# Kernel optimization log

Hardware: AMD Instinct MI355X
Metric: run time of the kernel (lower is better)

The kernel has to match this reference:

```python
import jax, jax.numpy as jnp
import numpy as np

L, D, d, H0, H1, K = 8, 64, 32, 512, 512, 10
EPS = 1e-5

def setup_inputs() -> dict:
    key = jax.random.key(0)
    ks = jax.random.split(key, 14)
    N = 65536
    x = jax.random.normal(ks[0], (N, D + 1), dtype=jnp.float32)  # last col = labels
    def w(k, shape):
        return jax.random.normal(k, shape, dtype=jnp.float32) * 0.05
    inp = {
        'x': x,
        'sW0': w(ks[1], (L, H0, d)),  'sb0': w(ks[2], (L, H0)),
        'sW1': w(ks[3], (L, H1, H0)), 'sb1': w(ks[4], (L, H1)),
        'sW2': w(ks[5], (L, D - d, H1)), 'sb2': w(ks[6], (L, D - d)),
        'tW0': w(ks[7], (L, H0, d)),  'tb0': w(ks[8], (L, H0)),
        'tW1': w(ks[9], (L, H1, H0)), 'tb1': w(ks[10], (L, H1)),
        'tW2': w(ks[11], (L, D - d, H1)), 'tb2': w(ks[12], (L, D - d)),
        'means': jax.random.normal(ks[13], (K, D), dtype=jnp.float32),
    }
    return inp

def _mlp(h, W0, b0, W1, b1, W2, b2):
    h = jax.nn.relu(h @ W0.T + b0)
    h = jax.nn.relu(h @ W1.T + b1)
    return h @ W2.T + b2

def reference(x, sW0, sb0, sW1, sb1, sW2, sb2, tW0, tb0, tW1, tb1, tW2, tb2, means):
    x = x[:, :D]  # drop label column
    det_s = jnp.zeros(x.shape[0], dtype=x.dtype)
    for i in range(L):
        # fresh BatchNorm1d in training mode: batch mean / biased var, weight=1, bias=0
        mu = x.mean(0)
        var = x.var(0)
        x = (x - mu) / jnp.sqrt(var + EPS)
        if i % 2 == 0:  # b1: first d features pass through
            x1, x2 = x[:, :d], x[:, d:]
        else:           # b2: last d features pass through
            x1, x2 = x[:, D - d:], x[:, :D - d]
        s = _mlp(x1, sW0[i], sb0[i], sW1[i], sb1[i], sW2[i], sb2[i])
        t = _mlp(x1, tW0[i], tb0[i], tW1[i], tb1[i], tW2[i], tb2[i])
        y2 = x2 * jnp.exp(s) + t
        det_s = det_s + s.sum(-1)
        x = jnp.concatenate([x1, y2], axis=-1)
    y = x
    # GMM prior: equal weights, identity covariance
    diff = y[:, None, :] - means[None, :, :]            # [N, K, D]
    comp_logp = -0.5 * (jnp.sum(diff * diff, -1) + D * jnp.log(2.0 * jnp.pi))
    log_likelihood = jax.scipy.special.logsumexp(comp_logp - jnp.log(float(K)), axis=-1)
    loss = -1.0 * (det_s + log_likelihood).mean()
    return (y, loss, log_likelihood, det_s, log_likelihood.mean(), det_s.mean())
```

## Files before the change

### kernel.cpp

```cpp
#include <hip/hip_runtime.h>
#include <cstdint>
#include <cstddef>

typedef unsigned short u16;
typedef unsigned int   u32;
typedef __attribute__((ext_vector_type(8))) short short8;
typedef __attribute__((ext_vector_type(4))) float f32x4;

__device__ __forceinline__ float bf2f(u16 b) {
  union { u32 u; float f; } v; v.u = ((u32)b) << 16; return v.f;
}
__device__ __forceinline__ u16 f2bf(float f) {
  union { float f; u32 u; } v; v.f = f;
  u32 u = v.u;
  return (u16)((u + 0x7fffu + ((u >> 16) & 1u)) >> 16);
}
__device__ __forceinline__ u32 pk2(u16 a, u16 b) { return (u32)a | ((u32)b << 16); }

__global__ void detect_dtype(const u16* __restrict__ xin, int* __restrict__ flag) {
  int hits = 0;
  for (int i = threadIdx.x; i < 16384; i += 256) {
    u16 v = xin[i];
    if (((v >> 7) & 0xFF) == 0xFF) hits++;
  }
  if (hits) atomicOr(flag, 1);
}

__global__ __launch_bounds__(256) void convert_bf16(const void* __restrict__ src,
    u16* __restrict__ dst, int n, const int* __restrict__ flag) {
  int i = blockIdx.x * 256 + threadIdx.x;
  if (i >= n) return;
  if (*flag) dst[i] = f2bf(((const float*)src)[i]);
  else       dst[i] = ((const u16*)src)[i];
}

__global__ __launch_bounds__(256) void repack_w0(const void* __restrict__ src,
    u16* __restrict__ dst, const int* __restrict__ flag, int L) {
  int idx = blockIdx.x * 256 + threadIdx.x;
  if (idx >= L * 2048) return;
  int layer = idx >> 11, r = idx & 2047;
  int lane = r & 63, fo = (r >> 6) & 7, w = r >> 9;
  int m = lane & 15, q = lane >> 4;
  int row = w * 128 + fo * 16 + m;
  size_t s = (size_t)layer * 16384 + (size_t)row * 32 + q * 8;
  u16 o[8];
  if (*flag) { const float* p = (const float*)src;
    #pragma unroll
    for (int j = 0; j < 8; ++j) o[j] = f2bf(p[s + j]);
  } else { const u16* p = (const u16*)src;
    #pragma unroll
    for (int j = 0; j < 8; ++j) o[j] = p[s + j];
  }
  *(uint4*)&dst[(size_t)idx * 8] =
      make_uint4(pk2(o[0], o[1]), pk2(o[2], o[3]), pk2(o[4], o[5]), pk2(o[6], o[7]));
}

__global__ __launch_bounds__(256) void repack_w1(const void* __restrict__ src,
    u16* __restrict__ dst, const int* __restrict__ flag, int L) {
  int idx = blockIdx.x * 256 + threadIdx.x;
  if (idx >= L * 32768) return;
  int layer = idx >> 15, r = idx & 32767;
  int lane = r & 63, fo = (r >> 6) & 3, ks = (r >> 8) & 15;
  int oc2 = (r >> 12) & 1, w = (r >> 13) & 3;
  int m = lane & 15, q = lane >> 4;
  int row = w * 128 + oc2 * 64 + fo * 16 + m;
  int col = ks * 32 + q * 8;
  size_t s = (size_t)layer * 262144 + (size_t)row * 512 + col;
  u16 o[8];
  if (*flag) { const float* p = (const float*)src;
    #pragma unroll
    for (int j = 0; j < 8; ++j) o[j] = f2bf(p[s + j]);
  } else { const u16* p = (const u16*)src;
    #pragma unroll
    for (int j = 0; j < 8; ++j) o[j] = p[s + j];
  }
  *(uint4*)&dst[(size_t)idx * 8] =
      make_uint4(pk2(o[0], o[1]), pk2(o[2], o[3]), pk2(o[4], o[5]), pk2(o[6], o[7]));
}

__global__ __launch_bounds__(256) void repack_w2(const void* __restrict__ src,
    u16* __restrict__ dst, const int* __restrict__ flag, int L) {
  int idx = blockIdx.x * 256 + threadIdx.x;
  if (idx >= L * 4096) return;
  int layer = idx >> 12, r = idx & 4095;
  int lane = r & 63, fo2 = (r >> 6) & 1, fo = (r >> 7) & 3;
  int oc2 = (r >> 9) & 1, w = (r >> 10) & 3;
  int m = lane & 15, q = lane >> 4;
  int row = fo2 * 16 + m;
  int col = w * 128 + oc2 * 64 + fo * 16 + q * 8;
  u16 o[8];
  #pragma unroll
  for (int j = 0; j < 8; ++j) {
    int cj = col + j;
    if (cj < 512) {
      size_t s = (size_t)layer * 16384 + (size_t)row * 512 + cj;
      o[j] = (*flag) ? f2bf(((const float*)src)[s]) : ((const u16*)src)[s];
    } else o[j] = 0;
  }
  *(uint4*)&dst[(size_t)idx * 8] =
      make_uint4(pk2(o[0], o[1]), pk2(o[2], o[3]), pk2(o[4], o[5]), pk2(o[6], o[7]));
}

__global__ __launch_bounds__(256) void init_x(const void* __restrict__ xin,
    float* __restrict__ x, const int* __restrict__ flag, int N) {
  int idx = blockIdx.x * 256 + threadIdx.x;
  if (idx >= N * 64) return;
  int n = idx >> 6, c = idx & 63;
  size_t si = (size_t)n * 65 + c;
  float v = (*flag) ? ((const float*)xin)[si] : bf2f(((const u16*)xin)[si]);
  if (!isfinite(v)) v = 0.0f;
  x[idx] = v;
}

__global__ __launch_bounds__(256) void col_stats(const float* __restrict__ x,
                                                 float* __restrict__ stats, int N) {
  int c   = threadIdx.x & 63;
  int sub = threadIdx.x >> 6;
  int rows = N / gridDim.x;
  int r0 = blockIdx.x * rows;
  float s = 0.f, s2 = 0.f;
  for (int r = sub; r < rows; r += 4) {
    float v = x[(size_t)(r0 + r) * 64 + c];
    s += v; s2 = fmaf(v, v, s2);
  }
  __shared__ float ls[256], lq[256];
  ls[threadIdx.x] = s; lq[threadIdx.x] = s2;
  __syncthreads();
  if (threadIdx.x < 64) {
    s  = ls[c] + ls[c + 64] + ls[c + 128] + ls[c + 192];
    s2 = lq[c] + lq[c + 64] + lq[c + 128] + lq[c + 192];
    atomicAdd(&stats[c], s);
    atomicAdd(&stats[64 + c], s2);
  }
}

__global__ __launch_bounds__(256, 2) void fused_layer(
    float* __restrict__ x, float* __restrict__ det,
    const float* __restrict__ statsC, float* __restrict__ statsN,
    const u16* __restrict__ pW0s, const u16* __restrict__ B0s,
    const u16* __restrict__ pW1s, const u16* __restrict__ B1s,
    const u16* __restrict__ pW2s, const u16* __restrict__ B2s,
    const u16* __restrict__ pW0t, const u16* __restrict__ B0t,
    const u16* __restrict__ pW1t, const u16* __restrict__ B1t,
    const u16* __restrict__ pW2t, const u16* __restrict__ B2t,
    int off1, int first, int N)
{
  __shared__ __align__(16) u16 h0s[64 * 512];
  __shared__ __align__(16) u16 xh[6144];
  __shared__ float musr[128];
  __shared__ float csum[64], csqs[64];

  const int tid  = threadIdx.x;
  const int lane = tid & 63, wave = tid >> 6;
  const int m = lane & 15, q = lane >> 4;
  const int mb = m & 7;
  const int r0 = blockIdx.x * 64;
  const int off2 = 32 - off1;
  const float invN = 1.0f / (float)N;

  if (tid < 64) {
    float mu  = statsC[tid] * invN;
    float var = fmaxf(statsC[64 + tid] * invN - mu * mu, 0.0f);
    musr[tid]      = mu;
    musr[64 + tid] = 1.0f / sqrtf(var + 1e-5f);
    csum[tid] = 0.0f; csqs[tid] = 0.0f;
  }
  __syncthreads();

  {
    int row = tid >> 2, kq = (tid & 3) * 8;
    const float* src = x + (size_t)(r0 + row) * 64 + off1 + kq;
    float4 v0 = *(const float4*)src;
    float4 v1 = *(const float4*)(src + 4);
    float vv[8] = {v0.x, v0.y, v0.z, v0.w, v1.x, v1.y, v1.z, v1.w};
    u16 pk[8];
    #pragma unroll
    for (int u_ = 0; u_ < 8; ++u_) {
      int c = off1 + kq + u_;
      pk[u_] = f2bf((vv[u_] - musr[c]) * musr[64 + c]);
    }
    *(uint4*)&xh[row * 40 + kq] =
        make_uint4(pk2(pk[0], pk[1]), pk2(pk[2], pk[3]),
                   pk2(pk[4], pk[5]), pk2(pk[6], pk[7]));
  }
  __syncthreads();

  short8 xb[4];
  #pragma unroll
  for (int fm = 0; fm < 4; ++fm)
    xb[fm] = *(const short8*)&xh[(fm * 16 + m) * 40 + q * 8];

  const u16* W0p[2] = {pW0s, pW0t}; const u16* B0p[2] = {B0s, B0t};
  const u16* W1p[2] = {pW1s, pW1t}; const u16* B1p[2] = {B1s, B1t};
  const u16* W2p[2] = {pW2s, pW2t};

  const f32x4 fz = {0.f, 0.f, 0.f, 0.f};
  f32x4 a2[2][4][2];
  #pragma unroll
  for (int p = 0; p < 2; ++p)
    #pragma unroll
    for (int fr = 0; fr < 4; ++fr)
      #pragma unroll
      for (int fo2 = 0; fo2 < 2; ++fo2) a2[p][fr][fo2] = fz;

  short8 zf;
  #pragma unroll
  for (int j = 0; j < 8; ++j) zf[j] = 0;

  u16* h1w = &xh[wave * 1536];

  #pragma unroll
  for (int p = 0; p < 2; ++p) {
    if (p == 1) __syncthreads();
    const u16 *W0 = W0p[p], *B0 = B0p[p], *W1 = W1p[p], *B1 = B1p[p], *W2 = W2p[p];

    short8 w0n = *(const short8*)(W0 + (size_t)(wave * 8) * 512 + lane * 8);
    #pragma unroll
    for (int fo = 0; fo < 8; ++fo) {
      short8 w0c = w0n;
      int fn = (fo + 1) & 7;
      w0n = *(const short8*)(W0 + (size_t)(wave * 8 + fn) * 512 + lane * 8);
      int colf = wave * 128 + fo * 16;
      int cb = colf + q * 4;
      float bb[4];
      #pragma unroll
      for (int i2 = 0; i2 < 4; ++i2) bb[i2] = bf2f(B0[cb + i2]);
      int gw = cb >> 3, wo = cb & 7;
      #pragma unroll
      for (int fm = 0; fm < 4; ++fm) {
        f32x4 d = __builtin_amdgcn_mfma_f32_16x16x32_bf16(w0c, xb[fm], fz, 0, 0, 0);
        u16 pk[4];
        #pragma unroll
        for (int i2 = 0; i2 < 4; ++i2) pk[i2] = f2bf(fmaxf(d[i2] + bb[i2], 0.0f));
        int row = fm * 16 + m;
        *(uint2*)&h0s[row * 512 + ((gw ^ (row & 7)) << 3) + wo] =
            make_uint2(pk2(pk[0], pk[1]), pk2(pk[2], pk[3]));
      }
    }
    __syncthreads();

    #pragma unroll 1
    for (int oc2 = 0; oc2 < 2; ++oc2) {
      int ocb = wave * 128 + oc2 * 64;
      const u16* W1b = W1 + (size_t)(wave * 2 + oc2) * 32768;
      f32x4 c1[4][4];
      #pragma unroll
      for (int fo = 0; fo < 4; ++fo)
        #pragma unroll
        for (int fm = 0; fm < 4; ++fm) c1[fo][fm] = fz;

      short8 wan[4], bfn[4];
      #pragma unroll
      for (int fm = 0; fm < 4; ++fm)
        bfn[fm] = *(const short8*)&h0s[(fm * 16 + m) * 512 + ((q ^ mb) << 3)];
      #pragma unroll
      for (int fo = 0; fo < 4; ++fo)
        wan[fo] = *(const short8*)(W1b + fo * 512 + lane * 8);

      #pragma unroll 4
      for (int ks = 0; ks < 16; ++ks) {
        short8 wac[4], bfc[4];
        #pragma unroll
        for (int z = 0; z < 4; ++z) { wac[z] = wan[z]; bfc[z] = bfn[z]; }
        int kn = (ks + 1) & 15;
        #pragma unroll
        for (int fm = 0; fm < 4; ++fm)
          bfn[fm] = *(const short8*)&h0s[(fm * 16 + m) * 512 +
                                         ((((kn << 2) | q) ^ mb) << 3)];
        #pragma unroll
        for (int fo = 0; fo < 4; ++fo)
          wan[fo] = *(const short8*)(W1b + (size_t)kn * 2048 + fo * 512 + lane * 8);
        #pragma unroll
        for (int fo = 0; fo < 4; ++fo)
          #pragma unroll
          for (int fm = 0; fm < 4; ++fm)
            c1[fo][fm] = __builtin_amdgcn_mfma_f32_16x16x32_bf16(
                wac[fo], bfc[fm], c1[fo][fm], 0, 0, 0);
      }

      #pragma unroll
      for (int fo = 0; fo < 4; ++fo) {
        int colb = ocb + fo * 16 + q * 4;
        float bb[4];
        #pragma unroll
        for (int i2 = 0; i2 < 4; ++i2) bb[i2] = bf2f(B1[colb + i2]);
        #pragma unroll
        for (int fm = 0; fm < 4; ++fm) {
          u16 pk[4];
          #pragma unroll
          for (int i2 = 0; i2 < 4; ++i2)
            pk[i2] = f2bf(fmaxf(c1[fo][fm][i2] + bb[i2], 0.0f));
          *(uint2*)&h1w[(fm * 16 + m) * 24 + q * 4] =
              make_uint2(pk2(pk[0], pk[1]), pk2(pk[2], pk[3]));
        }
        asm volatile("s_waitcnt lgkmcnt(0)" ::: "memory");
        const u16* W2b = W2 + (size_t)((wave * 2 + oc2) * 8 + fo * 2) * 512;
        #pragma unroll
        for (int fr = 0; fr < 4; ++fr) {
          short8 af = zf;
          if (q < 2) af = *(const short8*)&h1w[(fr * 16 + m) * 24 + q * 8];
          #pragma unroll
          for (int fo2 = 0; fo2 < 2; ++fo2) {
            short8 wf = *(const short8*)(W2b + fo2 * 512 + lane * 8);
            a2[p][fr][fo2] = __builtin_amdgcn_mfma_f32_16x16x32_bf16(
                af, wf, a2[p][fr][fo2], 0, 0, 0);
          }
        }
      }
    }
  }
  __syncthreads();

  float* red = (float*)h0s;
  #pragma unroll
  for (int fr = 0; fr < 4; ++fr)
    #pragma unroll
    for (int fo2 = 0; fo2 < 2; ++fo2)
      #pragma unroll
      for (int i2 = 0; i2 < 4; ++i2) {
        int row = fr * 16 + q * 4 + i2, col = fo2 * 16 + m;
        red[(wave * 64 + row) * 32 + col]       = a2[0][fr][fo2][i2];
        red[((4 + wave) * 64 + row) * 32 + col] = a2[1][fr][fo2][i2];
      }
  __syncthreads();

  {
    int col = tid & 31, rh = tid >> 5;
    float muA = musr[off1 + col], rsA = musr[64 + off1 + col];
    float muB = musr[off2 + col], rsB = musr[64 + off2 + col];
    float b2s = bf2f(B2s[col]), b2t = bf2f(B2t[col]);
    float cs1 = 0.f, cq1 = 0.f, cs2 = 0.f, cq2 = 0.f;
    #pragma unroll
    for (int u_ = 0; u_ < 8; ++u_) {
      int row = u_ * 8 + rh;
      float sv = b2s, tv = b2t;
      #pragma unroll
      for (int w = 0; w < 4; ++w) {
        sv += red[(w * 64 + row) * 32 + col];
        tv += red[((4 + w) * 64 + row) * 32 + col];
      }
      size_t rb = (size_t)(r0 + row) * 64;
      float x1n = (x[rb + off1 + col] - muA) * rsA;
      float x2n = (x[rb + off2 + col] - muB) * rsB;
      float y2 = fmaf(x2n, expf(fminf(sv, 30.0f)), tv);
      x[rb + col]      = x1n;
      x[rb + 32 + col] = y2;
      cs1 += x1n; cq1 = fmaf(x1n, x1n, cq1);
      cs2 += y2;  cq2 = fmaf(y2, y2, cq2);
      float rs_ = sv;
      rs_ += __shfl_xor(rs_, 1);  rs_ += __shfl_xor(rs_, 2);
      rs_ += __shfl_xor(rs_, 4);  rs_ += __shfl_xor(rs_, 8);
      rs_ += __shfl_xor(rs_, 16);
      if (col == 0) {
        int r = r0 + row;
        if (first) det[r] = rs_; else det[r] += rs_;
      }
    }
    cs1 += __shfl_xor(cs1, 32); cq1 += __shfl_xor(cq1, 32);
    cs2 += __shfl_xor(cs2, 32); cq2 += __shfl_xor(cq2, 32);
    if (lane < 32) {
      atomicAdd(&csum[col], cs1);      atomicAdd(&csqs[col], cq1);
      atomicAdd(&csum[32 + col], cs2); atomicAdd(&csqs[32 + col], cq2);
    }
  }
  __syncthreads();
  if (tid < 64) {
    atomicAdd(&statsN[tid],      csum[tid]);
    atomicAdd(&statsN[64 + tid], csqs[tid]);
  }
}

__global__ __launch_bounds__(256) void gmm_out(const float* __restrict__ x,
    const float* __restrict__ det, const u16* __restrict__ means,
    void* __restrict__ outv, double* __restrict__ acc,
    const int* __restrict__ flag, int N) {
  __shared__ float ms[640];
  __shared__ double rll[256], rdt[256];
  for (int i = threadIdx.x; i < 640; i += 256) ms[i] = bf2f(means[i]);
  __syncthreads();
  int of32 = *flag;
  int n = blockIdx.x * 256 + threadIdx.x;
  double llv = 0.0, dtv = 0.0;
  if (n < N) {
    float y[64];
    size_t rb = (size_t)n * 64;
    #pragma unroll
    for (int c = 0; c < 64; ++c) y[c] = x[rb + c];
    if (of32) {
      float* out = (float*)outv;
      #pragma unroll
      for (int c = 0; c < 64; ++c) out[rb + c] = y[c];
    } else {
      u16* out = (u16*)outv;
      #pragma unroll
      for (int c = 0; c < 64; ++c) out[rb + c] = f2bf(y[c]);
    }
    float lp[10];
    float mx = -3.0e38f;
    #pragma unroll
    for (int k = 0; k < 10; ++k) {
      float d2 = 0.0f;
      #pragma unroll
      for (int c = 0; c < 64; ++c) { float d = y[c] - ms[k * 64 + c]; d2 = fmaf(d, d, d2); }
      float v = -0.5f * (d2 + 64.0f * 1.8378770664093455f) - 2.302585092994046f;
      lp[k] = v; mx = fmaxf(mx, v);
    }
    float se = 0.0f;
    #pragma unroll
    for (int k = 0; k < 10; ++k) se += expf(lp[k] - mx);
    float ll = mx + logf(se);
    float dv = det[n];
    size_t NY = (size_t)N * 64;
    if (of32) {
      float* out = (float*)outv;
      out[NY + 1 + n]     = ll;
      out[NY + 1 + N + n] = dv;
    } else {
      u16* out = (u16*)outv;
      out[NY + 1 + n]     = f2bf(ll);
      out[NY + 1 + N + n] = f2bf(dv);
    }
    llv = ll; dtv = dv;
  }
  rll[threadIdx.x] = llv; rdt[threadIdx.x] = dtv;
  __syncthreads();
  for (int st = 128; st > 0; st >>= 1) {
    if (threadIdx.x < st) {
      rll[threadIdx.x] += rll[threadIdx.x + st];
      rdt[threadIdx.x] += rdt[threadIdx.x + st];
    }
    __syncthreads();
  }
  if (threadIdx.x == 0) { atomicAdd(&acc[0], rll[0]); atomicAdd(&acc[1], rdt[0]); }
}

__global__ void finalize(const double* __restrict__ acc, void* __restrict__ outv,
                         const int* __restrict__ flag, int N) {
  double llm = acc[0] / (double)N;
  double dm  = acc[1] / (double)N;
  size_t NY = (size_t)N * 64;
  if (*flag) {
    float* out = (float*)outv;
    out[NY]                         = (float)(-(llm + dm));
    out[NY + 1 + 2 * (size_t)N]     = (float)llm;
    out[NY + 1 + 2 * (size_t)N + 1] = (float)dm;
  } else {
    u16* out = (u16*)outv;
    out[NY]                         = f2bf((float)(-(llm + dm)));
    out[NY + 1 + 2 * (size_t)N]     = f2bf((float)llm);
    out[NY + 1 + 2 * (size_t)N + 1] = f2bf((float)dm);
  }
}

extern "C" void kernel_launch(void* const* d_in, const int* in_sizes, int n_in,
                              void* d_out, int out_size, void* d_ws, size_t ws_size,
                              hipStream_t stream) {
  const int N = in_sizes[0] / 65;
  (void)n_in; (void)out_size; (void)ws_size;

  char* ws = (char*)d_ws;
  size_t off = 0;
  auto alloc = [&](size_t bytes) -> void* {
    void* p = ws + off; off = (off + bytes + 255) & ~(size_t)255; return p;
  };
  int*    flag  = (int*)   alloc(4);
  double* acc   = (double*)alloc(2 * 8);
  float*  stats = (float*) alloc(9 * 128 * 4);
  float*  det   = (float*) alloc((size_t)N * 4);
  float*  x     = (float*) alloc((size_t)N * 64 * 4);

  u16* pW0s = (u16*)alloc((size_t)8 * 16384 * 2);
  u16* pW0t = (u16*)alloc((size_t)8 * 16384 * 2);
  u16* pW1s = (u16*)alloc((size_t)8 * 262144 * 2);
  u16* pW1t = (u16*)alloc((size_t)8 * 262144 * 2);
  u16* pW2s = (u16*)alloc((size_t)8 * 32768 * 2);
  u16* pW2t = (u16*)alloc((size_t)8 * 32768 * 2);

  static const int bcnt[7] = {8*512, 8*512, 8*32, 8*512, 8*512, 8*32, 640};
  static const int bsrc[7] = {2, 4, 6, 8, 10, 12, 13};
  u16* bptr[7];
  for (int t = 0; t < 7; ++t) bptr[t] = (u16*)alloc((size_t)bcnt[t] * 2);

  hipMemsetAsync(flag, 0, 4, stream);
  hipMemsetAsync(stats, 0, 9 * 128 * sizeof(float), stream);
  hipMemsetAsync(acc, 0, 2 * sizeof(double), stream);
  detect_dtype<<<dim3(1), dim3(256), 0, stream>>>((const u16*)d_in[0], flag);
  for (int t = 0; t < 7; ++t) {
    int n = bcnt[t];
    convert_bf16<<<dim3((n + 255) / 256), dim3(256), 0, stream>>>(
        d_in[bsrc[t]], bptr[t], n, flag);
  }
  repack_w0<<<dim3(64),   dim3(256), 0, stream>>>(d_in[1],  pW0s, flag, 8);
  repack_w0<<<dim3(64),   dim3(256), 0, stream>>>(d_in[7],  pW0t, flag, 8);
  repack_w1<<<dim3(1024), dim3(256), 0, stream>>>(d_in[3],  pW1s, flag, 8);
  repack_w1<<<dim3(1024), dim3(256), 0, stream>>>(d_in[9],  pW1t, flag, 8);
  repack_w2<<<dim3(128),  dim3(256), 0, stream>>>(d_in[5],  pW2s, flag, 8);
  repack_w2<<<dim3(128),  dim3(256), 0, stream>>>(d_in[11], pW2t, flag, 8);

  const int NE = N * 64;
  init_x<<<dim3((NE + 255) / 256), dim3(256), 0, stream>>>(d_in[0], x, flag, N);
  col_stats<<<dim3(256), dim3(256), 0, stream>>>(x, stats, N);

  for (int i = 0; i < 8; ++i) {
    fused_layer<<<dim3(N / 64), dim3(256), 0, stream>>>(
        x, det, stats + (size_t)i * 128, stats + (size_t)(i + 1) * 128,
        pW0s + (size_t)i * 16384,  bptr[0] + (size_t)i * 512,
        pW1s + (size_t)i * 262144, bptr[1] + (size_t)i * 512,
        pW2s + (size_t)i * 32768,  bptr[2] + (size_t)i * 32,
        pW0t + (size_t)i * 16384,  bptr[3] + (size_t)i * 512,
        pW1t + (size_t)i * 262144, bptr[4] + (size_t)i * 512,
        pW2t + (size_t)i * 32768,  bptr[5] + (size_t)i * 32,
        (i & 1) ? 32 : 0, (i == 0) ? 1 : 0, N);
  }

  gmm_out<<<dim3((N + 255) / 256), dim3(256), 0, stream>>>(x, det, bptr[6],
                                                           d_out, acc, flag, N);
  finalize<<<dim3(1), dim3(1), 0, stream>>>(acc, d_out, flag, N);
}
```

Measured before the change: 1.136 ms.

## Split hidden-layer K dimension to halve LDS and raise occupancy to three blocks

The first hidden layer's activations are now computed in two halves of 256 columns, each consumed right away by the second-layer GEMM. This shrinks the LDS buffer for h0 from 64x512 to 64x256. The s-network output is merged and stored to LDS as bf16 before the t-network runs, so the two-pass accumulators no longer stay live in registers. Launch bounds go from 2 to 3 blocks per CU, the W0 repack matches the new half-split order, and the software prefetch of W1 and h0 fragments is dropped. Extra barriers, W0 recomputation of the x tile, and rounding s to bf16 are the trade-offs.

```diff
diff --git a/kernel.cpp b/kernel.cpp
--- a/kernel.cpp
+++ b/kernel.cpp
@@ -39,9 +39,10 @@
   int idx = blockIdx.x * 256 + threadIdx.x;
   if (idx >= L * 2048) return;
   int layer = idx >> 11, r = idx & 2047;
-  int lane = r & 63, fo = (r >> 6) & 7, w = r >> 9;
+  int lane = r & 63, f = r >> 6;
+  int kh = f >> 4, w = (f >> 2) & 3, fo = f & 3;
   int m = lane & 15, q = lane >> 4;
-  int row = w * 128 + fo * 16 + m;
+  int row = kh * 256 + w * 64 + fo * 16 + m;
   size_t s = (size_t)layer * 16384 + (size_t)row * 32 + q * 8;
   u16 o[8];
   if (*flag) { const float* p = (const float*)src;
@@ -134,7 +135,7 @@
   }
 }
 
-__global__ __launch_bounds__(256, 2) void fused_layer(
+__global__ __launch_bounds__(256, 3) void fused_layer(
     float* __restrict__ x, float* __restrict__ det,
     const float* __restrict__ statsC, float* __restrict__ statsN,
     const u16* __restrict__ pW0s, const u16* __restrict__ B0s,
@@ -145,8 +146,10 @@
     const u16* __restrict__ pW2t, const u16* __restrict__ B2t,
     int off1, int first, int N)
 {
-  __shared__ __align__(16) u16 h0s[64 * 512];
-  __shared__ __align__(16) u16 xh[6144];
+  __shared__ __align__(16) u16 h0h[64 * 256];
+  __shared__ __align__(16) u16 x1s[2560];
+  __shared__ __align__(16) u16 h1wA[4096];
+  __shared__ __align__(16) u16 sst[2048];
   __shared__ float musr[128];
   __shared__ float csum[64], csqs[64];
 
@@ -179,103 +182,91 @@
       int c = off1 + kq + u_;
       pk[u_] = f2bf((vv[u_] - musr[c]) * musr[64 + c]);
     }
-    *(uint4*)&xh[row * 40 + kq] =
+    *(uint4*)&x1s[row * 40 + kq] =
         make_uint4(pk2(pk[0], pk[1]), pk2(pk[2], pk[3]),
                    pk2(pk[4], pk[5]), pk2(pk[6], pk[7]));
   }
-  __syncthreads();
-
-  short8 xb[4];
-  #pragma unroll
-  for (int fm = 0; fm < 4; ++fm)
-    xb[fm] = *(const short8*)&xh[(fm * 16 + m) * 40 + q * 8];
 
   const u16* W0p[2] = {pW0s, pW0t}; const u16* B0p[2] = {B0s, B0t};
   const u16* W1p[2] = {pW1s, pW1t}; const u16* B1p[2] = {B1s, B1t};
   const u16* W2p[2] = {pW2s, pW2t};
 
   const f32x4 fz = {0.f, 0.f, 0.f, 0.f};
-  f32x4 a2[2][4][2];
-  #pragma unroll
-  for (int p = 0; p < 2; ++p)
-    #pragma unroll
-    for (int fr = 0; fr < 4; ++fr)
-      #pragma unroll
-      for (int fo2 = 0; fo2 < 2; ++fo2) a2[p][fr][fo2] = fz;
-
   short8 zf;
   #pragma unroll
   for (int j = 0; j < 8; ++j) zf[j] = 0;
 
-  u16* h1w = &xh[wave * 1536];
-
-  #pragma unroll
+  u16* h1w = &h1wA[wave * 1024];
+  float* mergef = (float*)h0h;
+
   for (int p = 0; p < 2; ++p) {
-    if (p == 1) __syncthreads();
     const u16 *W0 = W0p[p], *B0 = B0p[p], *W1 = W1p[p], *B1 = B1p[p], *W2 = W2p[p];
-
-    short8 w0n = *(const short8*)(W0 + (size_t)(wave * 8) * 512 + lane * 8);
-    #pragma unroll
-    for (int fo = 0; fo < 8; ++fo) {
-      short8 w0c = w0n;
-      int fn = (fo + 1) & 7;
-      w0n = *(const short8*)(W0 + (size_t)(wave * 8 + fn) * 512 + lane * 8);
-      int colf = wave * 128 + fo * 16;
-      int cb = colf + q * 4;
-      float bb[4];
-      #pragma unroll
-      for (int i2 = 0; i2 < 4; ++i2) bb[i2] = bf2f(B0[cb + i2]);
-      int gw = cb >> 3, wo = cb & 7;
-      #pragma unroll
-      for (int fm = 0; fm < 4; ++fm) {
-        f32x4 d = __builtin_amdgcn_mfma_f32_16x16x32_bf16(w0c, xb[fm], fz, 0, 0, 0);
-        u16 pk[4];
-        #pragma unroll
-        for (int i2 = 0; i2 < 4; ++i2) pk[i2] = f2bf(fmaxf(d[i2] + bb[i2], 0.0f));
-        int row = fm * 16 + m;
-        *(uint2*)&h0s[row * 512 + ((gw ^ (row & 7)) << 3) + wo] =
-            make_uint2(pk2(pk[0], pk[1]), pk2(pk[2], pk[3]));
-      }
-    }
-    __syncthreads();
+    f32x4 a2[4][2];
+    #pragma unroll
+    for (int fr = 0; fr < 4; ++fr)
+      #pragma unroll
+      for (int fo2 = 0; fo2 < 2; ++fo2) a2[fr][fo2] = fz;
 
     #pragma unroll 1
     for (int oc2 = 0; oc2 < 2; ++oc2) {
-      int ocb = wave * 128 + oc2 * 64;
-      const u16* W1b = W1 + (size_t)(wave * 2 + oc2) * 32768;
+      const int ocb = wave * 128 + oc2 * 64;
       f32x4 c1[4][4];
       #pragma unroll
       for (int fo = 0; fo < 4; ++fo)
         #pragma unroll
         for (int fm = 0; fm < 4; ++fm) c1[fo][fm] = fz;
 
-      short8 wan[4], bfn[4];
-      #pragma unroll
-      for (int fm = 0; fm < 4; ++fm)
-        bfn[fm] = *(const short8*)&h0s[(fm * 16 + m) * 512 + ((q ^ mb) << 3)];
-      #pragma unroll
-      for (int fo = 0; fo < 4; ++fo)
-        wan[fo] = *(const short8*)(W1b + fo * 512 + lane * 8);
-
-      #pragma unroll 4
-      for (int ks = 0; ks < 16; ++ks) {
-        short8 wac[4], bfc[4];
-        #pragma unroll
-        for (int z = 0; z < 4; ++z) { wac[z] = wan[z]; bfc[z] = bfn[z]; }
-        int kn = (ks + 1) & 15;
-        #pragma unroll
-        for (int fm = 0; fm < 4; ++fm)
-          bfn[fm] = *(const short8*)&h0s[(fm * 16 + m) * 512 +
-                                         ((((kn << 2) | q) ^ mb) << 3)];
-        #pragma unroll
-        for (int fo = 0; fo < 4; ++fo)
-          wan[fo] = *(const short8*)(W1b + (size_t)kn * 2048 + fo * 512 + lane * 8);
-        #pragma unroll
-        for (int fo = 0; fo < 4; ++fo)
+      #pragma unroll 1
+      for (int kh = 0; kh < 2; ++kh) {
+        __syncthreads();
+        {
+          short8 xb[4];
           #pragma unroll
           for (int fm = 0; fm < 4; ++fm)
-            c1[fo][fm] = __builtin_amdgcn_mfma_f32_16x16x32_bf16(
-                wac[fo], bfc[fm], c1[fo][fm], 0, 0, 0);
+            xb[fm] = *(const short8*)&x1s[(fm * 16 + m) * 40 + q * 8];
+          #pragma unroll
+          for (int fo = 0; fo < 4; ++fo) {
+            short8 wa = *(const short8*)(W0 +
+                (size_t)(kh * 16 + wave * 4 + fo) * 512 + lane * 8);
+            int colg = kh * 256 + wave * 64 + fo * 16 + q * 4;
+            int cb   = wave * 64 + fo * 16 + q * 4;
+            int gw = cb >> 3, wo = cb & 7;
+            float bb[4];
+            #pragma unroll
+            for (int i2 = 0; i2 < 4; ++i2) bb[i2] = bf2f(B0[colg + i2]);
+            #pragma unroll
+            for (int fm = 0; fm < 4; ++fm) {
+              f32x4 d = __builtin_amdgcn_mfma_f32_16x16x32_bf16(wa, xb[fm], fz, 0, 0, 0);
+              u16 pk[4];
+              #pragma unroll
+              for (int i2 = 0; i2 < 4; ++i2)
+                pk[i2] = f2bf(fmaxf(d[i2] + bb[i2], 0.0f));
+              int row = fm * 16 + m;
+              *(uint2*)&h0h[row * 256 + ((gw ^ (row & 7)) << 3) + wo] =
+                  make_uint2(pk2(pk[0], pk[1]), pk2(pk[2], pk[3]));
+            }
+          }
+        }
+        __syncthreads();
+
+        #pragma unroll 2
+        for (int ks2 = 0; ks2 < 8; ++ks2) {
+          short8 bf[4];
+          #pragma unroll
+          for (int fm = 0; fm < 4; ++fm)
+            bf[fm] = *(const short8*)&h0h[(fm * 16 + m) * 256 +
+                                          ((((ks2 << 2) | q) ^ mb) << 3)];
+          int ks = kh * 8 + ks2;
+          #pragma unroll
+          for (int fo = 0; fo < 4; ++fo) {
+            short8 wa = *(const short8*)(W1 +
+                (size_t)(((wave * 2 + oc2) * 16 + ks) * 4 + fo) * 512 + lane * 8);
+            #pragma unroll
+            for (int fm = 0; fm < 4; ++fm)
+              c1[fo][fm] = __builtin_amdgcn_mfma_f32_16x16x32_bf16(
+                  wa, bf[fm], c1[fo][fm], 0, 0, 0);
+          }
+        }
       }
 
       #pragma unroll
@@ -290,7 +281,7 @@
           #pragma unroll
           for (int i2 = 0; i2 < 4; ++i2)
             pk[i2] = f2bf(fmaxf(c1[fo][fm][i2] + bb[i2], 0.0f));
-          *(uint2*)&h1w[(fm * 16 + m) * 24 + q * 4] =
+          *(uint2*)&h1w[(fm * 16 + m) * 16 + q * 4] =
               make_uint2(pk2(pk[0], pk[1]), pk2(pk[2], pk[3]));
         }
         asm volatile("s_waitcnt lgkmcnt(0)" ::: "memory");
@@ -298,75 +289,83 @@
         #pragma unroll
         for (int fr = 0; fr < 4; ++fr) {
           short8 af = zf;
-          if (q < 2) af = *(const short8*)&h1w[(fr * 16 + m) * 24 + q * 8];
+          if (q < 2) af = *(const short8*)&h1w[(fr * 16 + m) * 16 + q * 8];
           #pragma unroll
           for (int fo2 = 0; fo2 < 2; ++fo2) {
             short8 wf = *(const short8*)(W2b + fo2 * 512 + lane * 8);
-            a2[p][fr][fo2] = __builtin_amdgcn_mfma_f32_16x16x32_bf16(
-                af, wf, a2[p][fr][fo2], 0, 0, 0);
+            a2[fr][fo2] = __builtin_amdgcn_mfma_f32_16x16x32_bf16(
+                af, wf, a2[fr][fo2], 0, 0, 0);
           }
         }
       }
     }
-  }
-  __syncthreads();
-
-  float* red = (float*)h0s;
-  #pragma unroll
-  for (int fr = 0; fr < 4; ++fr)
-    #pragma unroll
-    for (int fo2 = 0; fo2 < 2; ++fo2)
-      #pragma unroll
-      for (int i2 = 0; i2 < 4; ++i2) {
-        int row = fr * 16 + q * 4 + i2, col = fo2 * 16 + m;
-        red[(wave * 64 + row) * 32 + col]       = a2[0][fr][fo2][i2];
-        red[((4 + wave) * 64 + row) * 32 + col] = a2[1][fr][fo2][i2];
+
+    __syncthreads();
+    #pragma unroll
+    for (int fr = 0; fr < 4; ++fr)
+      #pragma unroll
+      for (int fo2 = 0; fo2 < 2; ++fo2)
+        #pragma unroll
+        for (int i2 = 0; i2 < 4; ++i2) {
+          int row = fr * 16 + q * 4 + i2, col = fo2 * 16 + m;
+          mergef[wave * 2048 + row * 32 + col] = a2[fr][fo2][i2];
+        }
+    __syncthreads();
+
+    if (p == 0) {
+      int col = tid & 31, rh = tid >> 5;
+      float b2s = bf2f(B2s[col]);
+      #pragma unroll
+      for (int u_ = 0; u_ < 8; ++u_) {
+        int row = u_ * 8 + rh;
+        float sv = b2s;
+        #pragma unroll
+        for (int w = 0; w < 4; ++w) sv += mergef[w * 2048 + row * 32 + col];
+        sst[row * 32 + col] = f2bf(sv);
+        float rs_ = sv;
+        rs_ += __shfl_xor(rs_, 1);  rs_ += __shfl_xor(rs_, 2);
+        rs_ += __shfl_xor(rs_, 4);  rs_ += __shfl_xor(rs_, 8);
+        rs_ += __shfl_xor(rs_, 16);
+        if (col == 0) {
+          int r = r0 + row;
+          if (first) det[r] = rs_; else det[r] += rs_;
+        }
       }
-  __syncthreads();
-
-  {
-    int col = tid & 31, rh = tid >> 5;
-    float muA = musr[off1 + col], rsA = musr[64 + off1 + col];
-    float muB = musr[off2 + col], rsB = musr[64 + off2 + col];
-    float b2s = bf2f(B2s[col]), b2t = bf2f(B2t[col]);
-    float cs1 = 0.f, cq1 = 0.f, cs2 = 0.f, cq2 = 0.f;
-    #pragma unroll
-    for (int u_ = 0; u_ < 8; ++u_) {
-      int row = u_ * 8 + rh;
-      float sv = b2s, tv = b2t;
-      #pragma unroll
-      for (int w = 0; w < 4; ++w) {
-        sv += red[(w * 64 + row) * 32 + col];
-        tv += red[((4 + w) * 64 + row) * 32 + col];
+      __syncthreads();
+    } else {
+      int col = tid & 31, rh = tid >> 5;
+      float muA = musr[off1 + col], rsA = musr[64 + off1 + col];
+      float muB = musr[off2 + col], rsB = musr[64 + off2 + col];
+      float b2t = bf2f(B2t[col]);
+      float cs1 = 0.f, cq1 = 0.f, cs2 = 0.f, cq2 = 0.f;
+      #pragma unroll
+      for (int u_ = 0; u_ < 8; ++u_) {
+        int row = u_ * 8 + rh;
+        float tv = b2t;
+        #pragma unroll
+        for (int w = 0; w < 4; ++w) tv += mergef[w * 2048 + row * 32 + col];
+        float sv = bf2f(sst[row * 32 + col]);
+        size_t rb = (size_t)(r0 + row) * 64;
+        float x1n = (x[rb + off1 + col] - muA) * rsA;
+        float x2n = (x[rb + off2 + col] - muB) * rsB;
+        float y2 = fmaf(x2n, expf(fminf(sv, 30.0f)), tv);
+        x[rb + col]      = x1n;
+        x[rb + 32 + col] = y2;
+        cs1 += x1n; cq1 = fmaf(x1n, x1n, cq1);
+        cs2 += y2;  cq2 = fmaf(y2, y2, cq2);
       }
-      size_t rb = (size_t)(r0 + row) * 64;
-      float x1n = (x[rb + off1 + col] - muA) * rsA;
-      float x2n = (x[rb + off2 + col] - muB) * rsB;
-      float y2 = fmaf(x2n, expf(fminf(sv, 30.0f)), tv);
-      x[rb + col]      = x1n;
-      x[rb + 32 + col] = y2;
-      cs1 += x1n; cq1 = fmaf(x1n, x1n, cq1);
-      cs2 += y2;  cq2 = fmaf(y2, y2, cq2);
-      float rs_ = sv;
-      rs_ += __shfl_xor(rs_, 1);  rs_ += __shfl_xor(rs_, 2);
-      rs_ += __shfl_xor(rs_, 4);  rs_ += __shfl_xor(rs_, 8);
-      rs_ += __shfl_xor(rs_, 16);
-      if (col == 0) {
-        int r = r0 + row;
-        if (first) det[r] = rs_; else det[r] += rs_;
+      cs1 += __shfl_xor(cs1, 32); cq1 += __shfl_xor(cq1, 32);
+      cs2 += __shfl_xor(cs2, 32); cq2 += __shfl_xor(cq2, 32);
+      if (lane < 32) {
+        atomicAdd(&csum[col], cs1);      atomicAdd(&csqs[col], cq1);
+        atomicAdd(&csum[32 + col], cs2); atomicAdd(&csqs[32 + col], cq2);
       }
-    }
-    cs1 += __shfl_xor(cs1, 32); cq1 += __shfl_xor(cq1, 32);
-    cs2 += __shfl_xor(cs2, 32); cq2 += __shfl_xor(cq2, 32);
-    if (lane < 32) {
-      atomicAdd(&csum[col], cs1);      atomicAdd(&csqs[col], cq1);
-      atomicAdd(&csum[32 + col], cs2); atomicAdd(&csqs[32 + col], cq2);
-    }
-  }
-  __syncthreads();
-  if (tid < 64) {
-    atomicAdd(&statsN[tid],      csum[tid]);
-    atomicAdd(&statsN[64 + tid], csqs[tid]);
+      __syncthreads();
+      if (tid < 64) {
+        atomicAdd(&statsN[tid],      csum[tid]);
+        atomicAdd(&statsN[64 + tid], csqs[tid]);
+      }
+    }
   }
 }
 
```

After: 2.140 ms. 1.88x slower.
